# Kernel tuning notes

Measured on AMD Instinct MI355X. Metric: run time of the kernel, lower is better.

Reference implementation:

```python
import jax, jax.numpy as jnp
import numpy as np

N = 50000      # num nodes
DIN = 256
DOUT = 256
E = 400000     # edges per sign
NEG_SLOPE = 0.2  # LeakyReLU(0.2)


def setup_inputs() -> dict:
    key = jax.random.key(0)
    ks = jax.random.split(key, 12)
    p = lambda k, shp: jax.random.normal(k, shp, jnp.float32) * 0.05
    return {
        "node_reps": jax.random.normal(ks[0], (N, DIN), jnp.float32),
        "adj_pos": jax.random.randint(ks[1], (2, E), 0, N, dtype=jnp.int32),
        "adj_neg": jax.random.randint(ks[2], (2, E), 0, N, dtype=jnp.int32),
        "basis": p(ks[3], (2, DIN, DOUT)),        # num_bases=num_relations=2
        "att": p(ks[4], (2, 2)),
        "mapping_func": p(ks[5], (1, 2 * DOUT)),
        "bias": p(ks[6], (1, DOUT)),
        "theta1": p(ks[7], (DOUT, DOUT)),          # HGNN_conv 1 linear weight
        "b1": jnp.zeros((DOUT,), jnp.float32),
        "theta2": p(ks[8], (DOUT, DOUT)),          # HGNN_conv 2 linear weight
        "b2": jnp.zeros((DOUT,), jnp.float32),
    }


def reference(node_reps, adj_pos, adj_neg, basis, att, mapping_func, bias,
              theta1, b1, theta2, b2):
    # basis-decomposed relation weights: Wr[r] = sum_b att[r,b] * basis[b]
    Wr = (att @ basis.reshape(2, -1)).reshape(2, DIN, DOUT)
    h_pos = node_reps @ Wr[0]
    h_neg = node_reps @ Wr[1]
    # HGNN_conv feature transforms (linear + bias)
    h_pos = h_pos @ theta1 + b1
    h_neg = h_neg @ theta2 + b2

    # edge attention score: mapping_func . concat(h[src], h[dst])
    w_src = mapping_func[0, :DOUT]
    w_dst = mapping_func[0, DOUT:]
    e_pos = h_pos[adj_pos[0]] @ w_src + h_pos[adj_pos[1]] @ w_dst  # [E]
    e_neg = h_neg[adj_neg[0]] @ w_src + h_neg[adj_neg[1]] @ w_dst  # [E]
    e_all = jnp.concatenate([e_pos, e_neg])                         # [2E]
    coeff = jax.nn.sigmoid(jnp.where(e_all > 0, e_all, NEG_SLOPE * e_all))

    # symmetric degree normalization over the union graph
    rows_all = jnp.concatenate([adj_pos[0], adj_neg[0]])
    cols_all = jnp.concatenate([adj_pos[1], adj_neg[1]])
    deg = jnp.sqrt(jax.ops.segment_sum(
        jnp.ones_like(coeff), rows_all, num_segments=N))            # [N]
    coeff = coeff / (deg[rows_all] * deg[cols_all])

    # sparse aggregation (SpecialSpmm): out[r] += coeff_e * h[c]
    h_agg_pos = jax.ops.segment_sum(
        coeff[:E, None] * h_pos[adj_pos[1]], adj_pos[0], num_segments=N)
    h_agg_neg = jax.ops.segment_sum(
        coeff[E:, None] * h_neg[adj_neg[1]], adj_neg[0], num_segments=N)

    output = h_agg_pos - h_agg_neg + bias
    return (output, h_agg_pos, h_agg_neg)
```

## Files before the change

### kernel.cpp

```cpp
#include <hip/hip_runtime.h>

#define N_NODES 50000
#define NEDGE   400000
#define SB      512
#define NSB     ((N_NODES + SB - 1) / SB)
#define H8SCALE 128.0f

typedef __bf16 bf16x8 __attribute__((ext_vector_type(8)));
typedef float  f32x4  __attribute__((ext_vector_type(4)));
typedef float  f32x2  __attribute__((ext_vector_type(2)));
typedef unsigned short u16x8 __attribute__((ext_vector_type(8)));
typedef int    i32x2  __attribute__((ext_vector_type(2)));

#define GLDS16(gp, lp) \
  __builtin_amdgcn_global_load_lds((const __attribute__((address_space(1))) void*)(gp), \
                                   (__attribute__((address_space(3))) void*)(lp), 16, 0, 0)

static __device__ __forceinline__ unsigned short f2bf(float f) {
  unsigned u = __float_as_uint(f);
  unsigned r = (u + 0x7fffu + ((u >> 16) & 1u)) >> 16;
  return (unsigned short)r;
}
static __device__ __forceinline__ float bf2f(unsigned short v) {
  return __uint_as_float((unsigned)v << 16);
}

__global__ __launch_bounds__(256) void fused0_kernel(
    const float* __restrict__ basis, const float* __restrict__ att,
    const float* __restrict__ theta1, const float* __restrict__ theta2,
    const float* __restrict__ bias1, const float* __restrict__ bias2,
    unsigned short* __restrict__ Wt, float* __restrict__ biasvec,
    const float* __restrict__ node, unsigned short* __restrict__ A16,
    const int* __restrict__ adjp, const int* __restrict__ adjn,
    int* __restrict__ cntp, int* __restrict__ cntn) {
  const int b = blockIdx.x;
  if (b < 512) {
    const int r = b >> 8, k = b & 255;
    const int n = threadIdx.x;
    const float a0 = att[r * 2 + 0], a1 = att[r * 2 + 1];
    const float* th = (r == 0) ? theta1 : theta2;
    const float* b0 = basis + k * 256;
    const float* b1p = basis + 65536 + k * 256;
    float ac0 = 0.f, ac1 = 0.f, ac2 = 0.f, ac3 = 0.f;
    for (int j = 0; j < 256; j += 4) {
      const float w0 = a0 * b0[j + 0] + a1 * b1p[j + 0];
      const float w1 = a0 * b0[j + 1] + a1 * b1p[j + 1];
      const float w2 = a0 * b0[j + 2] + a1 * b1p[j + 2];
      const float w3 = a0 * b0[j + 3] + a1 * b1p[j + 3];
      ac0 += w0 * th[(j + 0) * 256 + n];
      ac1 += w1 * th[(j + 1) * 256 + n];
      ac2 += w2 * th[(j + 2) * 256 + n];
      ac3 += w3 * th[(j + 3) * 256 + n];
    }
    Wt[(size_t)(r * 256 + n) * 256 + k] = f2bf((ac0 + ac1) + (ac2 + ac3));
    if (k == 0) biasvec[r * 256 + n] = (r == 0) ? bias1[n] : bias2[n];
  } else if (b < 2560) {
    const long total = (long)N_NODES * 256 / 4;
    long idx = (long)(b - 512) * 256 + threadIdx.x;
    const long stride = 2048L * 256;
    for (; idx < total; idx += stride) {
      const f32x4 v = __builtin_nontemporal_load(&((const f32x4*)node)[idx]);
      ushort4 o;
      o.x = f2bf(v.x); o.y = f2bf(v.y); o.z = f2bf(v.z); o.w = f2bf(v.w);
      ((ushort4*)A16)[idx] = o;
    }
  } else {
    const int g = (b - 2560) * 256 + threadIdx.x;
    if (g < NEDGE) atomicAdd(&cntp[adjp[g]], 1);
    else if (g < 2 * NEDGE) atomicAdd(&cntn[adjn[g - NEDGE]], 1);
  }
}

__global__ __launch_bounds__(256) void gemm_kernel(
    const unsigned short* __restrict__ A,
    const unsigned short* __restrict__ Wt,
    const float* __restrict__ biasvec,
    const float* __restrict__ mapping,
    unsigned char* __restrict__ H8,
    float* __restrict__ sdbuf) {
  __shared__ unsigned short smem[128 * 136];
  unsigned short* sA = smem;
  unsigned short* sB = smem + 8192;
  const int tid = threadIdx.x;
  const int wave = tid >> 6, lane = tid & 63;
  const int wm = wave >> 1, wn = wave & 1;
  const int m0 = blockIdx.y * 128;
  const int n0 = blockIdx.x * 128;

  f32x4 acc[4][4];
#pragma unroll
  for (int a = 0; a < 4; ++a)
#pragma unroll
    for (int b = 0; b < 4; ++b) acc[a][b] = (f32x4){0.f, 0.f, 0.f, 0.f};

  const int srow = lane >> 3;
  const int skel = ((lane & 7) ^ srow) << 3;

  for (int ks = 0; ks < 4; ++ks) {
    const int kg = ks * 64 + skel;
#pragma unroll
    for (int c = 0; c < 4; ++c) {
      const int chunk = wave * 4 + c;
      const int row = chunk * 8 + srow;
      int rowg = m0 + row;
      rowg = rowg < N_NODES ? rowg : N_NODES - 1;
      GLDS16(A + (size_t)rowg * 256 + kg, sA + chunk * 512);
      GLDS16(Wt + (size_t)(n0 + row) * 256 + kg, sB + chunk * 512);
    }
    __syncthreads();
#pragma unroll
    for (int kk = 0; kk < 2; ++kk) {
      const int kb = (kk * 32 + ((lane >> 4) << 3)) << 1;
      bf16x8 af[4], bfr[4];
#pragma unroll
      for (int m16 = 0; m16 < 4; ++m16) {
        const int row = wm * 64 + m16 * 16 + (lane & 15);
        af[m16] = *(const bf16x8*)((const char*)sA + row * 128 + (kb ^ ((row & 7) << 4)));
      }
#pragma unroll
      for (int n16 = 0; n16 < 4; ++n16) {
        const int col = wn * 64 + n16 * 16 + (lane & 15);
        bfr[n16] = *(const bf16x8*)((const char*)sB + col * 128 + (kb ^ ((col & 7) << 4)));
      }
#pragma unroll
      for (int m16 = 0; m16 < 4; ++m16)
#pragma unroll
        for (int n16 = 0; n16 < 4; ++n16)
          acc[m16][n16] = __builtin_amdgcn_mfma_f32_16x16x32_bf16(af[m16], bfr[n16], acc[m16][n16], 0, 0, 0);
    }
    __syncthreads();
  }

  const bool sgn = (n0 >= 256);
  const int nb = (sgn ? (n0 - 256) : n0) >> 7;
  const int slice = nb * 2 + wn;
  float* __restrict__ sS = sdbuf + ((size_t)((sgn ? 2 : 0) + 0) * 4 + slice) * N_NODES;
  float* __restrict__ sD = sdbuf + ((size_t)((sgn ? 2 : 0) + 1) * 4 + slice) * N_NODES;
  float bv[4], wsv[4], wdv[4];
#pragma unroll
  for (int n16 = 0; n16 < 4; ++n16) {
    const int colg = n0 + wn * 64 + n16 * 16 + (lane & 15);
    bv[n16] = biasvec[colg];
    const int cm = colg & 255;
    wsv[n16] = mapping[cm];
    wdv[n16] = mapping[256 + cm];
  }
#pragma unroll
  for (int m16 = 0; m16 < 4; ++m16) {
    const int rowb = wm * 64 + m16 * 16 + ((lane >> 4) << 2);
#pragma unroll
    for (int j = 0; j < 4; ++j) {
      const int rowl = rowb + j;
      float vs = 0.f, vd = 0.f;
#pragma unroll
      for (int n16 = 0; n16 < 4; ++n16) {
        const float v = acc[m16][n16][j] + bv[n16];
        const int coll = wn * 64 + n16 * 16 + (lane & 15);
        smem[rowl * 136 + coll] = f2bf(v);
        vs += v * wsv[n16];
        vd += v * wdv[n16];
      }
#pragma unroll
      for (int off = 1; off < 16; off <<= 1) { vs += __shfl_xor(vs, off); vd += __shfl_xor(vd, off); }
      const int rowg = m0 + rowl;
      if ((lane & 15) == 0 && rowg < N_NODES) { sS[rowg] = vs; sD[rowg] = vd; }
    }
  }
  __syncthreads();
#pragma unroll
  for (int it = 0; it < 8; ++it) {
    const int row = it * 16 + (tid >> 4);
    const int c8 = (tid & 15) * 8;
    const int rowg = m0 + row;
    if (rowg < N_NODES) {
      const u16x8 v = *(const u16x8*)(smem + row * 136 + c8);
      float f[8];
#pragma unroll
      for (int q = 0; q < 8; ++q) f[q] = bf2f((unsigned short)v[q]) * H8SCALE;
      int w0 = __builtin_amdgcn_cvt_pk_fp8_f32(f[0], f[1], 0, false);
      w0     = __builtin_amdgcn_cvt_pk_fp8_f32(f[2], f[3], w0, true);
      int w1 = __builtin_amdgcn_cvt_pk_fp8_f32(f[4], f[5], 0, false);
      w1     = __builtin_amdgcn_cvt_pk_fp8_f32(f[6], f[7], w1, true);
      i32x2 o; o.x = w0; o.y = w1;
      *(i32x2*)(&H8[(size_t)rowg * 512 + n0 + c8]) = o;
    }
  }
}

__global__ __launch_bounds__(SB) void scan1_kernel(const int* __restrict__ cntp,
                                                   const int* __restrict__ cntn,
                                                   int* __restrict__ bsp, int* __restrict__ bsn) {
  __shared__ int lp[SB / 64], ln[SB / 64];
  const int i = blockIdx.x * SB + threadIdx.x;
  int vp = (i < N_NODES) ? cntp[i] : 0;
  int vn = (i < N_NODES) ? cntn[i] : 0;
#pragma unroll
  for (int off = 1; off < 64; off <<= 1) { vp += __shfl_xor(vp, off); vn += __shfl_xor(vn, off); }
  const int wave = threadIdx.x >> 6, lane = threadIdx.x & 63;
  if (lane == 0) { lp[wave] = vp; ln[wave] = vn; }
  __syncthreads();
  if (threadIdx.x == 0) {
    int ap = 0, an = 0;
#pragma unroll
    for (int w = 0; w < SB / 64; ++w) { ap += lp[w]; an += ln[w]; }
    bsp[blockIdx.x] = ap; bsn[blockIdx.x] = an;
  }
}

__global__ __launch_bounds__(SB) void scan3_kernel(const int* __restrict__ cntp,
                                                   const int* __restrict__ cntn,
                                                   const int* __restrict__ bsp,
                                                   const int* __restrict__ bsn,
                                                   const float* __restrict__ sdbuf,
                                                   int* __restrict__ rsp, int* __restrict__ rsn,
                                                   int* __restrict__ curp, int* __restrict__ curn,
                                                   f32x4* __restrict__ nip, f32x4* __restrict__ nin) {
  __shared__ int sp_[SB], sn_[SB];
  __shared__ int pbs[128], nbs[128];
  const int t = threadIdx.x;
  if (t < 128) {
    pbs[t] = (t < NSB) ? bsp[t] : 0;
    nbs[t] = (t < NSB) ? bsn[t] : 0;
  }
  __syncthreads();
  for (int off = 1; off < 128; off <<= 1) {
    const int ap = (t >= off && t < 128) ? pbs[t - off] : 0;
    const int an = (t >= off && t < 128) ? nbs[t - off] : 0;
    __syncthreads();
    if (t < 128) { pbs[t] += ap; nbs[t] += an; }
    __syncthreads();
  }
  const int basep = (blockIdx.x == 0) ? 0 : pbs[blockIdx.x - 1];
  const int basen = (blockIdx.x == 0) ? 0 : nbs[blockIdx.x - 1];
  if (blockIdx.x == 0 && t == 0) { rsp[N_NODES] = pbs[127]; rsn[N_NODES] = nbs[127]; }

  const int i = blockIdx.x * SB + t;
  const int cp = (i < N_NODES) ? cntp[i] : 0;
  const int cn = (i < N_NODES) ? cntn[i] : 0;
  sp_[t] = cp; sn_[t] = cn;
  __syncthreads();
  for (int off = 1; off < SB; off <<= 1) {
    const int ap = (t >= off) ? sp_[t - off] : 0;
    const int an = (t >= off) ? sn_[t - off] : 0;
    __syncthreads();
    sp_[t] += ap; sn_[t] += an;
    __syncthreads();
  }
  if (i < N_NODES) {
    const int rp = basep + sp_[t] - cp;
    const int rn = basen + sn_[t] - cn;
    rsp[i] = rp; curp[i] = rp;
    rsn[i] = rn; curn[i] = rn;
    const float rdeg = 1.f / sqrtf((float)(cp + cn));
    float sp4 = 0.f, dp4 = 0.f, sn4 = 0.f, dn4 = 0.f;
#pragma unroll
    for (int sl = 0; sl < 4; ++sl) {
      sp4 += sdbuf[(size_t)(0 * 4 + sl) * N_NODES + i];
      dp4 += sdbuf[(size_t)(1 * 4 + sl) * N_NODES + i];
      sn4 += sdbuf[(size_t)(2 * 4 + sl) * N_NODES + i];
      dn4 += sdbuf[(size_t)(3 * 4 + sl) * N_NODES + i];
    }
    nip[i] = (f32x4){sp4, dp4, rdeg, 0.f};
    nin[i] = (f32x4){sn4, dn4, rdeg, 0.f};
  }
}

__global__ void scatter_kernel(const int* __restrict__ adjp, const int* __restrict__ adjn,
                               const f32x4* __restrict__ nip, const f32x4* __restrict__ nin,
                               int* __restrict__ curp, int* __restrict__ curn,
                               i32x2* __restrict__ ecp, i32x2* __restrict__ ecn) {
  const int g = blockIdx.x * blockDim.x + threadIdx.x;
  if (g >= 2 * NEDGE) return;
  const bool neg = (g >= NEDGE);
  const int e2 = neg ? g - NEDGE : g;
  const int* __restrict__ adj = neg ? adjn : adjp;
  const f32x4* __restrict__ ni = neg ? nin : nip;
  int* __restrict__ cur = neg ? curn : curp;
  i32x2* __restrict__ ec = neg ? ecn : ecp;
  const int src = adj[e2], dst = adj[NEDGE + e2];
  const f32x4 a = ni[src], b = ni[dst];
  const float e = a.x + b.y;
  const float l = e > 0.f ? e : 0.2f * e;
  const float c = (1.f / (1.f + expf(-l))) * a.z * b.z * (1.0f / H8SCALE);
  const int p = atomicAdd(&cur[src], 1);
  i32x2 w; w.x = dst; w.y = __float_as_int(c);
  ec[p] = w;
}

__global__ __launch_bounds__(256) void agg_kernel(
    const unsigned char* __restrict__ H8,
    const int* __restrict__ rsp, const i32x2* __restrict__ ecp,
    const int* __restrict__ rsn, const i32x2* __restrict__ ecn,
    const float* __restrict__ bias, float* __restrict__ out) {
  __shared__ f32x4 sneg[2][64];
  const int wave = threadIdx.x >> 6, lane = threadIdx.x & 63;
  const int r = wave >> 1;
  const int sign = wave & 1;
  const int i = blockIdx.x * 2 + r;
  const int* __restrict__ rs  = sign ? rsn : rsp;
  const i32x2* __restrict__ ec = sign ? ecn : ecp;
  const unsigned char* __restrict__ Hb = H8 + sign * 256 + (size_t)lane * 4;
  const int beg = rs[i], end = rs[i + 1];
  f32x4 a0 = {0,0,0,0}, a1 = {0,0,0,0}, a2 = {0,0,0,0}, a3 = {0,0,0,0};
  for (int chunk = beg; chunk < end; chunk += 64) {
    const int m = (end - chunk < 64) ? end - chunk : 64;
    i32x2 ev = {0, 0};
    if (lane < m) ev = __builtin_nontemporal_load(&ec[chunk + lane]);
    const int   cv = ev.x;
    const float fv = __int_as_float(ev.y);
    int k = 0;
    for (; k + 4 <= m; k += 4) {
      const int   c0 = __shfl(cv, k),     c1 = __shfl(cv, k + 1);
      const int   c2 = __shfl(cv, k + 2), c3 = __shfl(cv, k + 3);
      const float f0 = __shfl(fv, k),     f1 = __shfl(fv, k + 1);
      const float f2 = __shfl(fv, k + 2), f3 = __shfl(fv, k + 3);
      const unsigned w0 = *(const unsigned*)(Hb + (size_t)c0 * 512);
      const unsigned w1 = *(const unsigned*)(Hb + (size_t)c1 * 512);
      const unsigned w2 = *(const unsigned*)(Hb + (size_t)c2 * 512);
      const unsigned w3 = *(const unsigned*)(Hb + (size_t)c3 * 512);
      const f32x2 l0 = __builtin_amdgcn_cvt_pk_f32_fp8(w0, false), h0 = __builtin_amdgcn_cvt_pk_f32_fp8(w0, true);
      const f32x2 l1 = __builtin_amdgcn_cvt_pk_f32_fp8(w1, false), h1 = __builtin_amdgcn_cvt_pk_f32_fp8(w1, true);
      const f32x2 l2 = __builtin_amdgcn_cvt_pk_f32_fp8(w2, false), h2 = __builtin_amdgcn_cvt_pk_f32_fp8(w2, true);
      const f32x2 l3 = __builtin_amdgcn_cvt_pk_f32_fp8(w3, false), h3 = __builtin_amdgcn_cvt_pk_f32_fp8(w3, true);
      a0.x += f0 * l0.x; a0.y += f0 * l0.y; a0.z += f0 * h0.x; a0.w += f0 * h0.y;
      a1.x += f1 * l1.x; a1.y += f1 * l1.y; a1.z += f1 * h1.x; a1.w += f1 * h1.y;
      a2.x += f2 * l2.x; a2.y += f2 * l2.y; a2.z += f2 * h2.x; a2.w += f2 * h2.y;
      a3.x += f3 * l3.x; a3.y += f3 * l3.y; a3.z += f3 * h3.x; a3.w += f3 * h3.y;
    }
    for (; k < m; ++k) {
      const int   c0 = __shfl(cv, k);
      const float f0 = __shfl(fv, k);
      const unsigned w0 = *(const unsigned*)(Hb + (size_t)c0 * 512);
      const f32x2 l0 = __builtin_amdgcn_cvt_pk_f32_fp8(w0, false), h0 = __builtin_amdgcn_cvt_pk_f32_fp8(w0, true);
      a0.x += f0 * l0.x; a0.y += f0 * l0.y; a0.z += f0 * h0.x; a0.w += f0 * h0.y;
    }
  }
  f32x4 a = (a0 + a1) + (a2 + a3);
  if (sign) sneg[r][lane] = a;
  __syncthreads();
  if (sign) {
    __builtin_nontemporal_store(a, ((f32x4*)(out + (size_t)2 * N_NODES * 256)) + (size_t)i * 64 + lane);
  } else {
    const f32x4 an = sneg[r][lane];
    const f32x4 bv = ((const f32x4*)bias)[lane];
    const f32x4 o = a - an + bv;
    __builtin_nontemporal_store(o, ((f32x4*)out) + (size_t)i * 64 + lane);
    __builtin_nontemporal_store(a, ((f32x4*)(out + (size_t)N_NODES * 256)) + (size_t)i * 64 + lane);
  }
}

extern "C" void kernel_launch(void* const* d_in, const int* in_sizes, int n_in,
                              void* d_out, int out_size, void* d_ws, size_t ws_size,
                              hipStream_t stream) {
  const float* node    = (const float*)d_in[0];
  const int*   adjp    = (const int*)d_in[1];
  const int*   adjn    = (const int*)d_in[2];
  const float* basis   = (const float*)d_in[3];
  const float* att     = (const float*)d_in[4];
  const float* mapping = (const float*)d_in[5];
  const float* bias    = (const float*)d_in[6];
  const float* theta1  = (const float*)d_in[7];
  const float* b1      = (const float*)d_in[8];
  const float* theta2  = (const float*)d_in[9];
  const float* b2      = (const float*)d_in[10];
  float* out = (float*)d_out;

  size_t off = 0;
  char* wsb = (char*)d_ws;
  auto alloc = [&](size_t bytes) -> char* {
    char* p = wsb + off;
    off = (off + bytes + 255) & ~(size_t)255;
    return p;
  };
  unsigned short* A16 = (unsigned short*)alloc((size_t)N_NODES * 256 * 2);
  unsigned char*  H8  = (unsigned char*)alloc((size_t)N_NODES * 512);
  unsigned short* Wt  = (unsigned short*)alloc(512 * 256 * 2);
  float* biasvec = (float*)alloc(512 * 4);
  float* sdbuf = (float*)alloc((size_t)16 * N_NODES * 4);
  f32x4* nip = (f32x4*)alloc((size_t)N_NODES * 16);
  f32x4* nin = (f32x4*)alloc((size_t)N_NODES * 16);
  int* cnt2 = (int*)alloc((size_t)2 * N_NODES * 4);
  int* cntp = cnt2, *cntn = cnt2 + N_NODES;
  int* cur2 = (int*)alloc((size_t)2 * N_NODES * 4);
  int* curp = cur2, *curn = cur2 + N_NODES;
  int* rsp = (int*)alloc((N_NODES + 1) * 4);
  int* rsn = (int*)alloc((N_NODES + 1) * 4);
  int* bsp = (int*)alloc(NSB * 4);
  int* bsn = (int*)alloc(NSB * 4);
  i32x2* ecp = (i32x2*)alloc((size_t)NEDGE * 8);
  i32x2* ecn = (i32x2*)alloc((size_t)NEDGE * 8);

  (void)hipMemsetAsync(cnt2, 0, (size_t)2 * N_NODES * 4, stream);

  fused0_kernel<<<512 + 2048 + (2 * NEDGE) / 256, 256, 0, stream>>>(
      basis, att, theta1, theta2, b1, b2, Wt, biasvec, node, A16, adjp, adjn, cntp, cntn);
  gemm_kernel<<<dim3(4, 391), 256, 0, stream>>>(A16, Wt, biasvec, mapping, H8, sdbuf);
  scan1_kernel<<<NSB, SB, 0, stream>>>(cntp, cntn, bsp, bsn);
  scan3_kernel<<<NSB, SB, 0, stream>>>(cntp, cntn, bsp, bsn, sdbuf, rsp, rsn, curp, curn, nip, nin);
  scatter_kernel<<<(2 * NEDGE) / 256, 256, 0, stream>>>(adjp, adjn, nip, nin, curp, curn, ecp, ecn);
  agg_kernel<<<N_NODES / 2, 256, 0, stream>>>(H8, rsp, ecp, rsn, ecn, bias, out);
}
```

Before: 210.8 us.

## Move edge coefficient computation into aggregation and swizzle GEMM blocks across XCDs

The scatter kernel now writes only destination column indices into CSR order. The attention coefficient (leaky-relu, sigmoid, degree normalization) is computed inside the aggregation kernel from per-node info, using the row's own entry and a gather of the neighbor's entry. This halves the CSR edge payload and removes the random gathers from scatter, at the cost of an extra random 16-byte gather per edge during aggregation. Separately, GEMM block indices are remapped so that consecutive tiles land on the same XCD, aiming for better L2 reuse of the A rows.

```diff
diff --git a/kernel.cpp b/kernel.cpp
--- a/kernel.cpp
+++ b/kernel.cpp
@@ -84,8 +84,12 @@
   const int tid = threadIdx.x;
   const int wave = tid >> 6, lane = tid & 63;
   const int wm = wave >> 1, wn = wave & 1;
-  const int m0 = blockIdx.y * 128;
-  const int n0 = blockIdx.x * 128;
+  const int bid = blockIdx.y * 4 + blockIdx.x;
+  const int xcd = bid & 7, loc = bid >> 3;
+  const int nq = 1564 >> 3, nr = 1564 & 7;
+  const int swz = (xcd < nr ? xcd * (nq + 1) : nr * (nq + 1) + (xcd - nr) * nq) + loc;
+  const int m0 = (swz >> 2) * 128;
+  const int n0 = (swz & 3) * 128;
 
   f32x4 acc[4][4];
 #pragma unroll
@@ -266,31 +270,25 @@
 }
 
 __global__ void scatter_kernel(const int* __restrict__ adjp, const int* __restrict__ adjn,
-                               const f32x4* __restrict__ nip, const f32x4* __restrict__ nin,
                                int* __restrict__ curp, int* __restrict__ curn,
-                               i32x2* __restrict__ ecp, i32x2* __restrict__ ecn) {
+                               int* __restrict__ colp, int* __restrict__ coln) {
   const int g = blockIdx.x * blockDim.x + threadIdx.x;
   if (g >= 2 * NEDGE) return;
-  const bool neg = (g >= NEDGE);
-  const int e2 = neg ? g - NEDGE : g;
-  const int* __restrict__ adj = neg ? adjn : adjp;
-  const f32x4* __restrict__ ni = neg ? nin : nip;
-  int* __restrict__ cur = neg ? curn : curp;
-  i32x2* __restrict__ ec = neg ? ecn : ecp;
-  const int src = adj[e2], dst = adj[NEDGE + e2];
-  const f32x4 a = ni[src], b = ni[dst];
-  const float e = a.x + b.y;
-  const float l = e > 0.f ? e : 0.2f * e;
-  const float c = (1.f / (1.f + expf(-l))) * a.z * b.z * (1.0f / H8SCALE);
-  const int p = atomicAdd(&cur[src], 1);
-  i32x2 w; w.x = dst; w.y = __float_as_int(c);
-  ec[p] = w;
+  if (g < NEDGE) {
+    const int src = adjp[g];
+    colp[atomicAdd(&curp[src], 1)] = adjp[NEDGE + g];
+  } else {
+    const int e2 = g - NEDGE;
+    const int src = adjn[e2];
+    coln[atomicAdd(&curn[src], 1)] = adjn[NEDGE + e2];
+  }
 }
 
 __global__ __launch_bounds__(256) void agg_kernel(
     const unsigned char* __restrict__ H8,
-    const int* __restrict__ rsp, const i32x2* __restrict__ ecp,
-    const int* __restrict__ rsn, const i32x2* __restrict__ ecn,
+    const int* __restrict__ rsp, const int* __restrict__ colp,
+    const int* __restrict__ rsn, const int* __restrict__ coln,
+    const f32x4* __restrict__ nip, const f32x4* __restrict__ nin,
     const float* __restrict__ bias, float* __restrict__ out) {
   __shared__ f32x4 sneg[2][64];
   const int wave = threadIdx.x >> 6, lane = threadIdx.x & 63;
@@ -298,16 +296,25 @@
   const int sign = wave & 1;
   const int i = blockIdx.x * 2 + r;
   const int* __restrict__ rs  = sign ? rsn : rsp;
-  const i32x2* __restrict__ ec = sign ? ecn : ecp;
+  const int* __restrict__ col = sign ? coln : colp;
+  const f32x4* __restrict__ ni = sign ? nin : nip;
   const unsigned char* __restrict__ Hb = H8 + sign * 256 + (size_t)lane * 4;
+  const f32x4 me = ni[i];
+  const float srow = me.x;
+  const float rdrow = me.z * (1.0f / H8SCALE);
   const int beg = rs[i], end = rs[i + 1];
   f32x4 a0 = {0,0,0,0}, a1 = {0,0,0,0}, a2 = {0,0,0,0}, a3 = {0,0,0,0};
   for (int chunk = beg; chunk < end; chunk += 64) {
     const int m = (end - chunk < 64) ? end - chunk : 64;
-    i32x2 ev = {0, 0};
-    if (lane < m) ev = __builtin_nontemporal_load(&ec[chunk + lane]);
-    const int   cv = ev.x;
-    const float fv = __int_as_float(ev.y);
+    int cv = 0;
+    float fv = 0.f;
+    if (lane < m) {
+      cv = __builtin_nontemporal_load(&col[chunk + lane]);
+      const f32x4 nb = ni[cv];
+      const float e = srow + nb.y;
+      const float l = e > 0.f ? e : 0.2f * e;
+      fv = (1.f / (1.f + expf(-l))) * rdrow * nb.z;
+    }
     int k = 0;
     for (; k + 4 <= m; k += 4) {
       const int   c0 = __shfl(cv, k),     c1 = __shfl(cv, k + 1);
@@ -387,8 +394,8 @@
   int* rsn = (int*)alloc((N_NODES + 1) * 4);
   int* bsp = (int*)alloc(NSB * 4);
   int* bsn = (int*)alloc(NSB * 4);
-  i32x2* ecp = (i32x2*)alloc((size_t)NEDGE * 8);
-  i32x2* ecn = (i32x2*)alloc((size_t)NEDGE * 8);
+  int* colp = (int*)alloc((size_t)NEDGE * 4);
+  int* coln = (int*)alloc((size_t)NEDGE * 4);
 
   (void)hipMemsetAsync(cnt2, 0, (size_t)2 * N_NODES * 4, stream);
 
@@ -397,6 +404,6 @@
   gemm_kernel<<<dim3(4, 391), 256, 0, stream>>>(A16, Wt, biasvec, mapping, H8, sdbuf);
   scan1_kernel<<<NSB, SB, 0, stream>>>(cntp, cntn, bsp, bsn);
   scan3_kernel<<<NSB, SB, 0, stream>>>(cntp, cntn, bsp, bsn, sdbuf, rsp, rsn, curp, curn, nip, nin);
-  scatter_kernel<<<(2 * NEDGE) / 256, 256, 0, stream>>>(adjp, adjn, nip, nin, curp, curn, ecp, ecn);
-  agg_kernel<<<N_NODES / 2, 256, 0, stream>>>(H8, rsp, ecp, rsn, ecn, bias, out);
-}
+  scatter_kernel<<<(2 * NEDGE) / 256, 256, 0, stream>>>(adjp, adjn, curp, curn, colp, coln);
+  agg_kernel<<<N_NODES / 2, 256, 0, stream>>>(H8, rsp, colp, rsn, coln, nip, nin, bias, out);
+}
```

New measurement: 213.3 us. No clear change (+1.2%).
